# Performance work log

Hardware: AMD Instinct MI355X
Metric: run time of the kernel (lower is better)

## Reference

```python
import jax, jax.numpy as jnp
import numpy as np

N_TOKENS = 2048
HIDDEN = 2880
N_HEADS = 64          # total query heads
N_KV = 8              # key/value heads
Q_MULT = N_HEADS // N_KV
HEAD_DIM = 64
SLIDING_WINDOW = 128  # layer_idx=0 -> sliding-window layer
SM_SCALE = 1.0 / np.sqrt(HEAD_DIM)
RMS_EPS = 1e-5
ROPE_BASE = 150000.0
ROPE_SCALING = 32.0
INIT_CTX = 4096
NTK_ALPHA = 1.0
NTK_BETA = 32.0


def _rope_tables(num_tokens):
    # YaRN NTK-by-parts inverse frequencies (static constants)
    freq = ROPE_BASE ** (np.arange(0, HEAD_DIM, 2, dtype=np.float64) / HEAD_DIM)
    concentration = 0.1 * np.log(ROPE_SCALING) + 1.0
    d_half = HEAD_DIM / 2
    low = d_half * np.log(INIT_CTX / (NTK_BETA * 2 * np.pi)) / np.log(ROPE_BASE)
    high = d_half * np.log(INIT_CTX / (NTK_ALPHA * 2 * np.pi)) / np.log(ROPE_BASE)
    interpolation = 1.0 / (ROPE_SCALING * freq)
    extrapolation = 1.0 / freq
    ramp = (np.arange(d_half) - low) / (high - low)
    m = 1.0 - np.clip(ramp, 0.0, 1.0)
    inv_freq = interpolation * (1.0 - m) + extrapolation * m
    t = np.arange(num_tokens, dtype=np.float64)
    freqs = np.outer(t, inv_freq)
    cos = jnp.asarray((np.cos(freqs) * concentration), dtype=jnp.float32)
    sin = jnp.asarray((np.sin(freqs) * concentration), dtype=jnp.float32)
    return cos, sin  # [num_tokens, HEAD_DIM//2]


def _apply_rotary(x, cos, sin):
    # x: [n, heads, HEAD_DIM]
    c = cos[:, None, :].astype(x.dtype)
    s = sin[:, None, :].astype(x.dtype)
    x1, x2 = jnp.split(x, 2, axis=-1)
    return jnp.concatenate([x1 * c - x2 * s, x2 * c + x1 * s], axis=-1)


def setup_inputs() -> dict:
    key = jax.random.key(0)
    ks = jax.random.split(key, 7)
    return {
        "x": jax.random.normal(ks[0], (N_TOKENS, HIDDEN), jnp.float32),
        "scale": jax.random.uniform(ks[1], (HIDDEN,), jnp.float32, 0.5, 1.5),
        "sink": jax.random.normal(ks[2], (N_HEADS,), jnp.float32),
        "w_qkv": jax.random.normal(ks[3], (HIDDEN, (N_HEADS + 2 * N_KV) * HEAD_DIM), jnp.float32) * 0.02,
        "b_qkv": jax.random.normal(ks[4], ((N_HEADS + 2 * N_KV) * HEAD_DIM,), jnp.float32) * 0.02,
        "w_o": jax.random.normal(ks[5], (N_HEADS * HEAD_DIM, HIDDEN), jnp.float32) * 0.02,
        "b_o": jax.random.normal(ks[6], (HIDDEN,), jnp.float32) * 0.02,
    }


def reference(x, scale, sink, w_qkv, b_qkv, w_o, b_o):
    n = x.shape[0]
    # RMSNorm (fp32)
    t = x.astype(jnp.float32)
    rms = jnp.sqrt(jnp.mean(t * t, axis=-1, keepdims=True) + RMS_EPS)
    t = (t / rms) * scale

    # QKV projection + split
    qkv = t @ w_qkv + b_qkv
    q_sz = N_HEADS * HEAD_DIM
    kv_sz = N_KV * HEAD_DIM
    q = qkv[:, :q_sz].reshape(n, N_HEADS, HEAD_DIM)
    k = qkv[:, q_sz:q_sz + kv_sz].reshape(n, N_KV, HEAD_DIM)
    v = qkv[:, q_sz + kv_sz:].reshape(n, N_KV, HEAD_DIM)

    # RoPE (YaRN)
    cos, sin = _rope_tables(n)
    q = _apply_rotary(q, cos, sin)
    k = _apply_rotary(k, cos, sin)

    # GQA layout: [n, N_KV, Q_MULT, HEAD_DIM]
    qg = q.reshape(n, N_KV, Q_MULT, HEAD_DIM)

    # scores: [N_KV, Q_MULT, n_q, n_kv]
    scores = jnp.einsum('nhgd,mhd->hgnm', qg, k) * SM_SCALE

    # causal + sliding-window mask
    q_pos = jnp.arange(n)[:, None]
    kv_pos = jnp.arange(n)[None, :]
    mask = jnp.where(kv_pos > q_pos, -jnp.inf, 0.0)
    mask = mask + jnp.where((SLIDING_WINDOW > 0) & (q_pos - kv_pos > SLIDING_WINDOW), -jnp.inf, 0.0)
    scores = scores + mask[None, None, :, :].astype(scores.dtype)

    # sink logit appended as extra softmax column, then dropped
    s_col = jnp.broadcast_to(sink.reshape(N_KV, Q_MULT, 1, 1), (N_KV, Q_MULT, n, 1))
    w = jax.nn.softmax(jnp.concatenate([scores, s_col], axis=-1), axis=-1)[..., :-1]

    attn = jnp.einsum('hgnm,mhd->nhgd', w, v).reshape(n, N_HEADS * HEAD_DIM)
    out = attn @ w_o + b_o
    return x + out


if __name__ == '__main__':
    inp = setup_inputs()
    y = reference(**inp)
    print(y.shape, y.dtype)
```

## Files before the change

### kernel.cpp

```cpp
#include <hip/hip_runtime.h>
#include <cstdint>
#include <cstddef>

#define HIDDEN   2880
#define QKV_N    5120
#define OPROJ_K  4096
#define NTOK     2048
#define WIN      128
#define SM_SCALE 0.125f

typedef _Float16 half8  __attribute__((ext_vector_type(8)));
typedef _Float16 half4v __attribute__((ext_vector_type(4)));
typedef float    f32x4  __attribute__((ext_vector_type(4)));

__device__ __forceinline__ void gload16(const void* g, void* l) {
  __builtin_amdgcn_global_load_lds((__attribute__((address_space(1))) void*)g,
                                   (__attribute__((address_space(3))) void*)l,
                                   16, 0, 0);
}

__device__ __forceinline__ _Float16 f2h(float f) { return (_Float16)f; }

#define NB_T0  (80 * 45)
#define NB_T1  (46 * 64)
#define NB_ROPE 256

__device__ __forceinline__ void cast_transpose64(const float* __restrict__ W,
                                                 _Float16* __restrict__ Wt,
                                                 int K, int N, int n0, int k0,
                                                 float* tile ) {
  int t = threadIdx.x;
  #pragma unroll
  for (int p = 0; p < 16; ++p) {
    int r = p * 4 + (t >> 6), cc = t & 63;
    float vv = 0.f;
    if (n0 + cc < N) vv = W[(size_t)(k0 + r) * N + n0 + cc];
    tile[r * 65 + cc] = vv;
  }
  __syncthreads();
  #pragma unroll
  for (int p = 0; p < 2; ++p) {
    int idx = p * 256 + t;
    int r = idx >> 3, ch = (idx & 7) * 8;
    half8 h;
    #pragma unroll
    for (int u = 0; u < 8; ++u) h[u] = (_Float16)tile[(ch + u) * 65 + r];
    *(half8*)&Wt[(size_t)(n0 + r) * K + k0 + ch] = h;
  }
}

__global__ __launch_bounds__(256) void prep_kernel(const float* __restrict__ x,
                                                   const float* __restrict__ scale,
                                                   const float* __restrict__ w_qkv,
                                                   const float* __restrict__ w_o,
                                                   _Float16* __restrict__ a_h,
                                                   _Float16* __restrict__ wtq,
                                                   _Float16* __restrict__ wto,
                                                   float2* __restrict__ tab) {
  __shared__ float smem[64 * 65];
  int b = blockIdx.x, t = threadIdx.x;
  if (b < NB_T0) {
    cast_transpose64(w_qkv, wtq, HIDDEN, QKV_N, (b % 80) * 64, (b / 80) * 64, smem);
    return;
  }
  b -= NB_T0;
  if (b < NB_T1) {
    cast_transpose64(w_o, wto, OPROJ_K, HIDDEN, (b % 46) * 64, (b / 46) * 64, smem);
    return;
  }
  b -= NB_T1;
  if (b < NTOK) {
    int row = b;
    const float4* xr = (const float4*)(x + (size_t)row * HIDDEN);
    const float4* sc = (const float4*)scale;
    float4 v0 = xr[t];
    float4 v1 = xr[t + 256];
    float4 v2 = (t < 208) ? xr[t + 512] : make_float4(0.f, 0.f, 0.f, 0.f);
    float ss = v0.x*v0.x + v0.y*v0.y + v0.z*v0.z + v0.w*v0.w
             + v1.x*v1.x + v1.y*v1.y + v1.z*v1.z + v1.w*v1.w
             + v2.x*v2.x + v2.y*v2.y + v2.z*v2.z + v2.w*v2.w;
    #pragma unroll
    for (int m = 1; m < 64; m <<= 1) ss += __shfl_xor(ss, m, 64);
    if ((t & 63) == 0) smem[t >> 6] = ss;
    __syncthreads();
    float inv = 1.0f / sqrtf((smem[0] + smem[1] + smem[2] + smem[3]) * (1.0f / HIDDEN) + 1e-5f);
    _Float16* orow = a_h + (size_t)row * HIDDEN;
    auto store4 = [&](int c4, const float4& v, const float4& s) {
      half4v h;
      h[0] = f2h(v.x * inv * s.x); h[1] = f2h(v.y * inv * s.y);
      h[2] = f2h(v.z * inv * s.z); h[3] = f2h(v.w * inv * s.w);
      *(half4v*)(orow + (size_t)c4 * 4) = h;
    };
    store4(t, v0, sc[t]);
    store4(t + 256, v1, sc[t + 256]);
    if (t < 208) store4(t + 512, v2, sc[t + 512]);
    return;
  }
  b -= NTOK;
  {
    int idx = b * 256 + t;
    int tok = idx >> 5, d = idx & 31;
    const double PI = 3.14159265358979323846;
    double i = (double)d;
    double lf = log(150000.0);
    double freq = exp(lf * (i / 32.0));
    double interp = 1.0 / (32.0 * freq);
    double extrap = 1.0 / freq;
    double low  = 32.0 * log(4096.0 / (32.0 * 2.0 * PI)) / lf;
    double high = 32.0 * log(4096.0 / (2.0 * PI)) / lf;
    double ramp = (i - low) / (high - low);
    double mm = 1.0 - fmin(fmax(ramp, 0.0), 1.0);
    double invf = interp * (1.0 - mm) + extrap * mm;
    double ang = (double)tok * invf;
    double conc = 0.1 * log(32.0) + 1.0;
    tab[idx] = make_float2((float)(cos(ang) * conc), (float)(sin(ang) * conc));
  }
}

template <int BM, bool QKV_MODE, int MINW>
__global__ __launch_bounds__(256, MINW) void gemm_kernel(const _Float16* __restrict__ A,
                                                         const _Float16* __restrict__ Bt,
                                                         const float* __restrict__ bias,
                                                         const float* __restrict__ resid,
                                                         const float2* __restrict__ tab,
                                                         void* __restrict__ Cout,
                                                         int M, int N, int K) {
  constexpr int MI = BM / 32;
  constexpr int NA = BM / 32;
  __shared__ _Float16 Alds[BM * 64];
  __shared__ _Float16 Blds[128 * 64];
  int tid = threadIdx.x;
  int wave = tid >> 6, lane = tid & 63;
  int wm = wave >> 1, wn = wave & 1;
  int c = lane & 15, quad = lane >> 4;
  int m0 = blockIdx.y * BM, n0 = blockIdx.x * 128;

  const _Float16* gAp[NA]; _Float16* lAp[NA];
  #pragma unroll
  for (int i = 0; i < NA; ++i) {
    int p = wave * 64 + i * 256 + lane;
    int r = p >> 3;
    int kl = (p & 7) ^ (r & 7);
    gAp[i] = A + (size_t)(m0 + r) * K + kl * 8;
    lAp[i] = Alds + (size_t)(wave * 64 + i * 256) * 8;
  }
  const _Float16* gBp[4]; _Float16* lBp[4];
  #pragma unroll
  for (int i = 0; i < 4; ++i) {
    int p = wave * 64 + i * 256 + lane;
    int r = p >> 3;
    int kl = (p & 7) ^ (r & 7);
    gBp[i] = Bt + (size_t)(n0 + r) * K + kl * 8;
    lBp[i] = Blds + (size_t)(wave * 64 + i * 256) * 8;
  }

  int px[2];
  px[0] = ((0 * 4 + quad) ^ (c & 7)) * 8;
  px[1] = ((1 * 4 + quad) ^ (c & 7)) * 8;

  f32x4 acc[MI][4] = {};
  int nIter = K >> 6;
  for (int kt = 0; kt < nIter; ++kt) {
    __syncthreads();
    #pragma unroll
    for (int i = 0; i < NA; ++i) { gload16(gAp[i], lAp[i]); gAp[i] += 64; }
    #pragma unroll
    for (int i = 0; i < 4; ++i)  { gload16(gBp[i], lBp[i]); gBp[i] += 64; }
    __syncthreads();
    half8 a[MI][2], b[4][2];
    #pragma unroll
    for (int i = 0; i < MI; ++i) {
      int row = wm * (BM / 2) + i * 16 + c;
      a[i][0] = *(const half8*)&Alds[row * 64 + px[0]];
      a[i][1] = *(const half8*)&Alds[row * 64 + px[1]];
    }
    #pragma unroll
    for (int j = 0; j < 4; ++j) {
      int row = wn * 64 + j * 16 + c;
      b[j][0] = *(const half8*)&Blds[row * 64 + px[0]];
      b[j][1] = *(const half8*)&Blds[row * 64 + px[1]];
    }
    #pragma unroll
    for (int i = 0; i < MI; ++i)
      #pragma unroll
      for (int j = 0; j < 4; ++j) {
        acc[i][j] = __builtin_amdgcn_mfma_f32_16x16x32_f16(a[i][0], b[j][0], acc[i][j], 0, 0, 0);
        acc[i][j] = __builtin_amdgcn_mfma_f32_16x16x32_f16(a[i][1], b[j][1], acc[i][j], 0, 0, 0);
      }
  }

  if (QKV_MODE) {
    _Float16* outp = (_Float16*)Cout;
    bool ropeTile = (n0 < 4608);
    #pragma unroll
    for (int i = 0; i < MI; ++i) {
      int rowb = m0 + wm * (BM / 2) + i * 16 + quad * 4;
      if (ropeTile) {
        #pragma unroll
        for (int jp = 0; jp < 2; ++jp) {
          int col = n0 + wn * 64 + jp * 16 + c;
          float b1 = bias[col], b2 = bias[col + 32];
          #pragma unroll
          for (int r = 0; r < 4; ++r) {
            float2 cs = tab[(size_t)(rowb + r) * 32 + jp * 16 + c];
            float x1 = acc[i][jp][r] + b1;
            float x2 = acc[i][jp + 2][r] + b2;
            outp[(size_t)(rowb + r) * QKV_N + col]      = f2h(x1 * cs.x - x2 * cs.y);
            outp[(size_t)(rowb + r) * QKV_N + col + 32] = f2h(x2 * cs.x + x1 * cs.y);
          }
        }
      } else {
        #pragma unroll
        for (int j = 0; j < 4; ++j) {
          int col = n0 + wn * 64 + j * 16 + c;
          float bv = bias[col];
          #pragma unroll
          for (int r = 0; r < 4; ++r)
            outp[(size_t)(rowb + r) * QKV_N + col] = f2h(acc[i][j][r] + bv);
        }
      }
    }
  } else {
    float* outp = (float*)Cout;
    #pragma unroll
    for (int i = 0; i < MI; ++i) {
      int rowb = m0 + wm * (BM / 2) + i * 16 + quad * 4;
      #pragma unroll
      for (int j = 0; j < 4; ++j) {
        int col = n0 + wn * 64 + j * 16 + c;
        if (col < N) {
          float bv = bias[col];
          #pragma unroll
          for (int r = 0; r < 4; ++r)
            outp[(size_t)(rowb + r) * N + col] =
                acc[i][j][r] + bv + resid[(size_t)(rowb + r) * N + col];
        }
      }
    }
  }
}

#define TQ 16
__global__ __launch_bounds__(256) void attn_kernel(const _Float16* __restrict__ qkv,
                                                   const float* __restrict__ sink,
                                                   _Float16* __restrict__ attn_out) {
  __shared__ __align__(16) char smem[61440];
  _Float16* Klds = (_Float16*)smem;
  _Float16* Qlds = (_Float16*)(smem + 20480);
  _Float16* Ps   = (_Float16*)smem;
  _Float16* Vt   = (_Float16*)(smem + 40960);

  int qt = blockIdx.x, kvh = blockIdx.y;
  int Q0 = qt * TQ;
  int kmin = (Q0 >= WIN) ? Q0 - WIN : 0;
  int nkv = Q0 + TQ - kmin;
  int tid = threadIdx.x;
  int wave = tid >> 6, lane = tid & 63;
  int c = lane & 15, quad = lane >> 4;

  {
    const _Float16* kbase = qkv + 4096 + kvh * 64;
    #pragma unroll
    for (int p = 0; p < 5; ++p) {
      int ci = p * 256 + wave * 64 + lane;
      int row = ci >> 3, pc = ci & 7;
      int lc = pc ^ (row & 7);
      gload16(kbase + (size_t)(kmin + row) * QKV_N + lc * 8,
              (char*)Klds + (size_t)(p * 256 + wave * 64) * 16);
    }
  }
  {
    const _Float16* qbase = qkv + kvh * 512;
    #pragma unroll
    for (int p = 0; p < 4; ++p) {
      int ci = p * 256 + wave * 64 + lane;
      int tok = ci >> 6, Lp = ci & 63;
      int Llog = (Lp & 56) | ((Lp ^ tok) & 7);
      gload16(qbase + (size_t)(Q0 + tok) * QKV_N + Llog * 8,
              (char*)Qlds + (size_t)(p * 256 + wave * 64) * 16);
    }
  }
  #pragma unroll
  for (int p = 0; p < 5; ++p) {
    int cc = p * 256 + tid;
    int col = cc % 160;
    int d0 = (cc / 160) * 8;
    union { uint4 u4; _Float16 hv[8]; } buf;
    if (col < nkv) buf.u4 = *(const uint4*)(qkv + (size_t)(kmin + col) * QKV_N + 4608 + kvh * 64 + d0);
    else           buf.u4 = make_uint4(0, 0, 0, 0);
    #pragma unroll
    for (int uu = 0; uu < 8; ++uu) Vt[(d0 + uu) * 160 + col] = buf.hv[uu];
  }

  __syncthreads();

  half8 aq[2][2];
  #pragma unroll
  for (int i = 0; i < 2; ++i) {
    int qm = wave * 2 + i;
    #pragma unroll
    for (int ks = 0; ks < 2; ++ks) {
      int kc = ks * 4 + quad;
      int Lp = qm * 8 + (kc ^ (c & 7));
      aq[i][ks] = *(const half8*)&Qlds[c * 512 + Lp * 8];
    }
  }

  f32x4 sacc[2][9] = {};
  #pragma unroll
  for (int j = 0; j < 9; ++j) {
    #pragma unroll
    for (int ks = 0; ks < 2; ++ks) {
      int kc = ks * 4 + quad;
      int pc = kc ^ (c & 7);
      half8 bk = *(const half8*)&Klds[(j * 16 + c) * 64 + pc * 8];
      #pragma unroll
      for (int i = 0; i < 2; ++i)
        sacc[i][j] = __builtin_amdgcn_mfma_f32_16x16x32_f16(aq[i][ks], bk, sacc[i][j], 0, 0, 0);
    }
  }

  __syncthreads();

  #pragma unroll
  for (int p = 0; p < 8; ++p) {
    int idx = p * 256 + tid;
    Ps[(idx >> 4) * 160 + 144 + (idx & 15)] = (_Float16)0.f;
  }

  #pragma unroll
  for (int i = 0; i < 2; ++i) {
    int qm = wave * 2 + i;
    float sk = sink[kvh * 8 + qm];
    #pragma unroll
    for (int r = 0; r < 4; ++r) {
      int qpos = Q0 + quad * 4 + r;
      float sv[9]; float mx = -3e38f;
      #pragma unroll
      for (int j = 0; j < 9; ++j) {
        int key = kmin + j * 16 + c;
        float s = sacc[i][j][r] * SM_SCALE;
        bool valid = (key <= qpos) && (qpos - key <= WIN);
        sv[j] = valid ? s : -3e38f;
        mx = fmaxf(mx, sv[j]);
      }
      #pragma unroll
      for (int msk = 1; msk < 16; msk <<= 1) mx = fmaxf(mx, __shfl_xor(mx, msk, 64));
      mx = fmaxf(mx, sk);
      float sum = 0.f; float pv[9];
      #pragma unroll
      for (int j = 0; j < 9; ++j) { float p = __expf(sv[j] - mx); pv[j] = p; sum += p; }
      #pragma unroll
      for (int msk = 1; msk < 16; msk <<= 1) sum += __shfl_xor(sum, msk, 64);
      sum += __expf(sk - mx);
      float inv = 1.0f / sum;
      int mrow = qm * 16 + quad * 4 + r;
      #pragma unroll
      for (int j = 0; j < 9; ++j)
        Ps[mrow * 160 + j * 16 + c] = f2h(pv[j] * inv);
    }
  }

  __syncthreads();

  f32x4 oacc[2][4] = {};
  #pragma unroll
  for (int ks = 0; ks < 5; ++ks) {
    half8 ap[2], bv[4];
    #pragma unroll
    for (int i = 0; i < 2; ++i)
      ap[i] = *(const half8*)&Ps[((wave * 2 + i) * 16 + c) * 160 + ks * 32 + quad * 8];
    #pragma unroll
    for (int j = 0; j < 4; ++j)
      bv[j] = *(const half8*)&Vt[(j * 16 + c) * 160 + ks * 32 + quad * 8];
    #pragma unroll
    for (int i = 0; i < 2; ++i)
      #pragma unroll
      for (int j = 0; j < 4; ++j)
        oacc[i][j] = __builtin_amdgcn_mfma_f32_16x16x32_f16(ap[i], bv[j], oacc[i][j], 0, 0, 0);
  }

  #pragma unroll
  for (int i = 0; i < 2; ++i) {
    int qm = wave * 2 + i;
    #pragma unroll
    for (int j = 0; j < 4; ++j)
      #pragma unroll
      for (int r = 0; r < 4; ++r) {
        int token = Q0 + quad * 4 + r;
        attn_out[(size_t)token * 4096 + (kvh * 8 + qm) * 64 + j * 16 + c] = f2h(oacc[i][j][r]);
      }
  }
}

extern "C" void kernel_launch(void* const* d_in, const int* in_sizes, int n_in,
                              void* d_out, int out_size, void* d_ws, size_t ws_size,
                              hipStream_t stream) {
  (void)in_sizes; (void)n_in; (void)out_size; (void)ws_size;
  const float* x      = (const float*)d_in[0];
  const float* scale  = (const float*)d_in[1];
  const float* sink   = (const float*)d_in[2];
  const float* w_qkv  = (const float*)d_in[3];
  const float* b_qkv  = (const float*)d_in[4];
  const float* w_o    = (const float*)d_in[5];
  const float* b_o    = (const float*)d_in[6];
  float* out = (float*)d_out;

  char* ws = (char*)d_ws;
  size_t off = 0;
  auto alloc = [&](size_t bytes) { void* p = ws + off; off += (bytes + 255) & ~(size_t)255; return p; };
  _Float16* wtq   = (_Float16*)alloc((size_t)QKV_N * HIDDEN * 2);
  _Float16* wto   = (_Float16*)alloc((size_t)2944 * OPROJ_K * 2);
  _Float16* a_h   = (_Float16*)alloc((size_t)NTOK * HIDDEN * 2);
  _Float16* qkv_h = (_Float16*)alloc((size_t)NTOK * QKV_N * 2);
  float2*   tab   = (float2*)alloc((size_t)NTOK * 32 * sizeof(float2));
  _Float16* at_h  = (_Float16*)wtq;

  int prep_blocks = NB_T0 + NB_T1 + NTOK + NB_ROPE;
  prep_kernel<<<prep_blocks, 256, 0, stream>>>(x, scale, w_qkv, w_o, a_h, wtq, wto, tab);
  gemm_kernel<128, true, 3><<<dim3(QKV_N / 128, NTOK / 128), 256, 0, stream>>>(
      a_h, wtq, b_qkv, nullptr, tab, qkv_h, NTOK, QKV_N, HIDDEN);
  attn_kernel<<<dim3(NTOK / TQ, 8), 256, 0, stream>>>(qkv_h, sink, at_h);
  gemm_kernel<64, false, 4><<<dim3(23, NTOK / 64), 256, 0, stream>>>(
      at_h, wto, b_o, x, nullptr, out, NTOK, HIDDEN, OPROJ_K);
}
```

Measured before the change: 333.4 us.

## Replace QKV GEMM with 8-wave 128x320 tile kernel with fused bias and RoPE

Adds a dedicated QKV projection kernel that uses 512 threads and a 128x320 output tile. It double-buffers A and B in 112KB of dynamic LDS through direct global-to-LDS loads, and splits each K step into two MFMA halves so the next prefetch overlaps the second half. The epilogue stages fp32 results in LDS and applies bias and RoPE per head before writing fp16. The larger tile raises arithmetic intensity and cuts the block count, at the cost of heavy LDS use that limits occupancy and a grid of 16x16 blocks that may not fill the GPU evenly.

```diff
diff --git a/kernel.cpp b/kernel.cpp
--- a/kernel.cpp
+++ b/kernel.cpp
@@ -114,6 +114,142 @@
     double ang = (double)tok * invf;
     double conc = 0.1 * log(32.0) + 1.0;
     tab[idx] = make_float2((float)(cos(ang) * conc), (float)(sin(ang) * conc));
+  }
+}
+
+#define QBM 128
+#define QBN 320
+
+__global__ __launch_bounds__(512, 2) void qkv8_kernel(const _Float16* __restrict__ A,
+                                                      const _Float16* __restrict__ Bt,
+                                                      const float* __restrict__ bias,
+                                                      const float2* __restrict__ tab,
+                                                      _Float16* __restrict__ out,
+                                                      int K) {
+  extern __shared__ char smem[];
+  int tid = threadIdx.x;
+  int wave = tid >> 6, lane = tid & 63;
+  int wm = wave >> 2, wn = wave & 3;
+  int c = lane & 15, quad = lane >> 4;
+  int n0 = blockIdx.x * QBN, m0 = blockIdx.y * QBM;
+  int NT = K >> 6;
+
+  const _Float16* gA[2];
+  #pragma unroll
+  for (int i = 0; i < 2; ++i) {
+    int ci = i * 512 + tid, r = ci >> 3, lc = (ci & 7) ^ (r & 7);
+    gA[i] = A + (size_t)(m0 + r) * K + lc * 8;
+  }
+  const _Float16* gB[5];
+  #pragma unroll
+  for (int i = 0; i < 5; ++i) {
+    int ci = i * 512 + tid, r = ci >> 3, lc = (ci & 7) ^ (r & 7);
+    gB[i] = Bt + (size_t)(n0 + r) * K + lc * 8;
+  }
+  char* lA = smem + (size_t)(wave * 64) * 16;
+  char* lB = smem + 32768 + (size_t)(wave * 64) * 16;
+
+  auto STAGE = [&](int sel, int t) {
+    size_t ko = (size_t)t * 64;
+    #pragma unroll
+    for (int i = 0; i < 2; ++i) gload16(gA[i] + ko, lA + sel * 16384 + i * 8192);
+    #pragma unroll
+    for (int i = 0; i < 5; ++i) gload16(gB[i] + ko, lB + sel * 40960 + i * 8192);
+  };
+
+  int aoff[2], boff[2];
+  #pragma unroll
+  for (int ks = 0; ks < 2; ++ks) {
+    int px = ((ks * 4 + quad) ^ (c & 7)) * 16;
+    aoff[ks] = (wm * 64 + c) * 128 + px;
+    boff[ks] = (wn * 80 + c) * 128 + px;
+  }
+
+  f32x4 acc[4][5] = {};
+  STAGE(0, 0);
+  STAGE(1, 1);
+
+  #pragma unroll 1
+  for (int t = 0; t < NT; ++t) {
+    if (t + 1 < NT) asm volatile("s_waitcnt vmcnt(7)" ::: "memory");
+    else            asm volatile("s_waitcnt vmcnt(0)" ::: "memory");
+    __builtin_amdgcn_s_barrier();
+    asm volatile("" ::: "memory");
+    const char* Ab = smem + (t & 1) * 16384;
+    const char* Bb = smem + 32768 + (t & 1) * 40960;
+    half8 a[4][2], b[5][2];
+    #pragma unroll
+    for (int i = 0; i < 4; ++i) {
+      a[i][0] = *(const half8*)(Ab + aoff[0] + i * 2048);
+      a[i][1] = *(const half8*)(Ab + aoff[1] + i * 2048);
+    }
+    #pragma unroll
+    for (int j = 0; j < 5; ++j) {
+      b[j][0] = *(const half8*)(Bb + boff[0] + j * 2048);
+      b[j][1] = *(const half8*)(Bb + boff[1] + j * 2048);
+    }
+    __builtin_amdgcn_s_setprio(1);
+    #pragma unroll
+    for (int j = 0; j < 5; ++j)
+      #pragma unroll
+      for (int i = 0; i < 4; ++i)
+        acc[i][j] = __builtin_amdgcn_mfma_f32_16x16x32_f16(a[i][0], b[j][0], acc[i][j], 0, 0, 0);
+    __builtin_amdgcn_s_setprio(0);
+    asm volatile("s_waitcnt lgkmcnt(0)" ::: "memory");
+    __builtin_amdgcn_s_barrier();
+    asm volatile("" ::: "memory");
+    if (t + 2 < NT) STAGE(t & 1, t + 2);
+    __builtin_amdgcn_s_setprio(1);
+    #pragma unroll
+    for (int j = 0; j < 5; ++j)
+      #pragma unroll
+      for (int i = 0; i < 4; ++i)
+        acc[i][j] = __builtin_amdgcn_mfma_f32_16x16x32_f16(a[i][1], b[j][1], acc[i][j], 0, 0, 0);
+    __builtin_amdgcn_s_setprio(0);
+  }
+
+  asm volatile("s_waitcnt lgkmcnt(0)" ::: "memory");
+  __builtin_amdgcn_s_barrier();
+  asm volatile("" ::: "memory");
+  float* fP = (float*)smem;
+  #pragma unroll
+  for (int h = 0; h < 2; ++h) {
+    if (wm == h) {
+      #pragma unroll
+      for (int j = 0; j < 5; ++j) {
+        int coll = wn * 80 + j * 16 + c;
+        float bv = bias[n0 + coll];
+        #pragma unroll
+        for (int i = 0; i < 4; ++i) {
+          int rowl = i * 16 + quad * 4;
+          #pragma unroll
+          for (int r = 0; r < 4; ++r)
+            fP[(rowl + r) * 324 + coll] = acc[i][j][r] + bv;
+        }
+      }
+    }
+    asm volatile("s_waitcnt lgkmcnt(0)" ::: "memory");
+    __builtin_amdgcn_s_barrier();
+    asm volatile("" ::: "memory");
+    #pragma unroll
+    for (int p = 0; p < 20; ++p) {
+      int idx = p * 512 + tid;
+      int row = idx / 160, s = idx - row * 160;
+      int head = s >> 5, d = s & 31;
+      int coll = head * 64 + d;
+      int gcol = n0 + coll;
+      int grow = m0 + h * 64 + row;
+      float x1 = fP[row * 324 + coll];
+      float x2 = fP[row * 324 + coll + 32];
+      float2 cs = (gcol < 4608) ? tab[(size_t)grow * 32 + d] : make_float2(1.f, 0.f);
+      out[(size_t)grow * QKV_N + gcol]      = f2h(x1 * cs.x - x2 * cs.y);
+      out[(size_t)grow * QKV_N + gcol + 32] = f2h(x2 * cs.x + x1 * cs.y);
+    }
+    if (h == 0) {
+      asm volatile("s_waitcnt lgkmcnt(0)" ::: "memory");
+      __builtin_amdgcn_s_barrier();
+      asm volatile("" ::: "memory");
+    }
   }
 }
 
@@ -416,10 +552,17 @@
   float2*   tab   = (float2*)alloc((size_t)NTOK * 32 * sizeof(float2));
   _Float16* at_h  = (_Float16*)wtq;
 
+  static int qkv_attr_set = 0;
+  if (!qkv_attr_set) {
+    hipFuncSetAttribute((const void*)qkv8_kernel,
+                        hipFuncAttributeMaxDynamicSharedMemorySize, 114688);
+    qkv_attr_set = 1;
+  }
+
   int prep_blocks = NB_T0 + NB_T1 + NTOK + NB_ROPE;
   prep_kernel<<<prep_blocks, 256, 0, stream>>>(x, scale, w_qkv, w_o, a_h, wtq, wto, tab);
-  gemm_kernel<128, true, 3><<<dim3(QKV_N / 128, NTOK / 128), 256, 0, stream>>>(
-      a_h, wtq, b_qkv, nullptr, tab, qkv_h, NTOK, QKV_N, HIDDEN);
+  qkv8_kernel<<<dim3(QKV_N / QBN, NTOK / QBM), 512, 114688, stream>>>(
+      a_h, wtq, b_qkv, tab, qkv_h, HIDDEN);
   attn_kernel<<<dim3(NTOK / TQ, 8), 256, 0, stream>>>(qkv_h, sink, at_h);
   gemm_kernel<64, false, 4><<<dim3(23, NTOK / 64), 256, 0, stream>>>(
       at_h, wto, b_o, x, nullptr, out, NTOK, HIDDEN, OPROJ_K);
```

New measurement: 338.3 us. About the same (+1.4%).
